# Optimization experiments

Hardware: AMD Instinct MI355X
Metric: run time of the kernel (lower is better)

The kernel has to match this reference:

```python
import math
import jax, jax.numpy as jnp
import numpy as np

B_, C_, K_, P_, STRIDE, ITERS = 32, 32, 3, 4, 2, 3
PSIZE = P_ * P_
EPS = 1e-8
LAM = 1e-3


def _unfold(x):
    # crude_convolution2d: gather-based unfold. x: (b, h, w, c)
    b, h, w, c = x.shape
    oh = int((h - K_ + 1) / STRIDE)
    idxs = np.array([[hi + k for k in range(K_)] for hi in range(0, h - K_ + 1, STRIDE)])  # (oh, K)
    x = x[:, idxs, :, :]        # (b, oh, K, w, c)
    x = x[:, :, :, idxs, :]     # (b, oh, K, ow, K, c)
    x = jnp.transpose(x, (0, 1, 3, 2, 4, 5))  # (b, oh, ow, K, K, c)
    return x, oh, oh


def _em_routing(v, a_in, beta_a, beta_u):
    # v: (n, Bk, C, psize), a_in: (n, Bk, 1). Standard matrix-capsule EM routing.
    n, Bk, C, psize = v.shape
    r = jnp.full((n, Bk, C), 1.0 / C, dtype=v.dtype)
    mu = a_out = None
    for it in range(ITERS):
        # M-step
        rr = r * a_in
        rr = rr / (jnp.sum(rr, axis=2, keepdims=True) + EPS)
        r_sum = jnp.sum(rr, axis=1, keepdims=True)              # (n, 1, C)
        coeff = (rr / (r_sum + EPS))[..., None]                 # (n, Bk, C, 1)
        mu = jnp.sum(coeff * v, axis=1, keepdims=True)          # (n, 1, C, psize)
        sigma_sq = jnp.sum(coeff * (v - mu) ** 2, axis=1, keepdims=True) + EPS
        log_sigma = 0.5 * jnp.log(sigma_sq)                     # log(sqrt(sigma_sq))
        cost_h = (beta_u[None, None, :, None] + log_sigma) * r_sum[..., None]
        a_out = jax.nn.sigmoid(LAM * (beta_a[None, None, :] - jnp.sum(cost_h, axis=3)))  # (n,1,C)
        if it < ITERS - 1:
            # E-step: Gaussian log-likelihood + log activation -> softmax over C
            ln_p = -(v - mu) ** 2 / (2.0 * sigma_sq) - log_sigma - 0.5 * math.log(2.0 * math.pi)
            ln_ap = jnp.sum(ln_p, axis=3) + jnp.log(a_out)      # (n, Bk, C)
            r = jax.nn.softmax(ln_ap, axis=2)
    return jnp.squeeze(mu, axis=1), jnp.squeeze(a_out, axis=1)


def setup_inputs() -> dict:
    key = jax.random.key(0)
    k1, k2 = jax.random.split(key)
    x = jax.random.uniform(k1, (8, 16, 16, B_ * (PSIZE + 1)), dtype=jnp.float32)
    weights = jax.random.normal(k2, (1, K_ * K_ * B_, C_, P_, P_), dtype=jnp.float32)
    beta_a = jnp.zeros((C_,), dtype=jnp.float32)
    beta_u = jnp.zeros((C_,), dtype=jnp.float32)
    return {"x": x, "weights": weights, "beta_a": beta_a, "beta_u": beta_u}


def reference(x, weights, beta_a, beta_u):
    b, h, w, c = x.shape
    xu, oh, ow = _unfold(x)                                   # (b, oh, ow, K, K, c)
    n = b * oh * ow
    p_in = xu[..., : B_ * PSIZE].reshape(n, K_ * K_ * B_, P_, P_)
    a_in = xu[..., B_ * PSIZE :].reshape(n, K_ * K_ * B_, 1)
    # transform_view: per (input-capsule k, output-capsule c) pose matmul
    v = jnp.einsum("nkij,kcjl->nkcil", p_in, weights[0]).reshape(n, K_ * K_ * B_, C_, PSIZE)
    mu, a_out = _em_routing(v, a_in, beta_a, beta_u)
    p_out = mu.reshape(b, oh, ow, C_ * PSIZE)
    a_out = a_out.reshape(b, oh, ow, C_)
    return jnp.concatenate([p_out, a_out], axis=3)
```

## Files before the change

kernel.cpp:

```cpp
#include <hip/hip_runtime.h>
#include <math.h>


#define NTH 512
#define KK 288
#define KSG 16
#define KT 18
#define CC 32
#define PS 16
#define EPSF 1e-8f
#define LAMF 1e-3f
#define HL2PI 0.91893853320467274178f
#define LOG2E 1.4426950408889634f

typedef float v2f __attribute__((ext_vector_type(2)));

__device__ __forceinline__ float4 ld4(const float* p){ return *(const float4*)p; }
__device__ __forceinline__ float rcpf(float x){ return __builtin_amdgcn_rcpf(x); }
__device__ __forceinline__ v2f bc2(float s){ return (v2f){s, s}; }
__device__ __forceinline__ v2f fma2(v2f a, v2f b, v2f c){ return __builtin_elementwise_fma(a, b, c); }

template<int CTRL>
__device__ __forceinline__ float dpp_add(float x){
  const int p = __builtin_amdgcn_update_dpp(0, __builtin_bit_cast(int, x),
                                            CTRL, 0xF, 0xF, true);
  return x + __builtin_bit_cast(float, p);
}
template<int CTRL>
__device__ __forceinline__ float dpp_max(float x){
  const int p = __builtin_amdgcn_update_dpp(0, __builtin_bit_cast(int, x),
                                            CTRL, 0xF, 0xF, true);
  return fmaxf(x, __builtin_bit_cast(float, p));
}
__device__ __forceinline__ float sum32(float s){
  s = dpp_add<0xB1>(s); s = dpp_add<0x4E>(s);
  s = dpp_add<0x141>(s); s = dpp_add<0x140>(s);
  s += __shfl_xor(s, 16);
  return s;
}

extern "C" __global__ void __launch_bounds__(NTH)
convcaps_em_kernel(const float* __restrict__ x, const float* __restrict__ wgt,
                   const float* __restrict__ beta_a, const float* __restrict__ beta_u,
                   float* __restrict__ out)
{
  __shared__ float sP[KK*PS];
  __shared__ float sA[KK];
  __shared__ float sPart[8*CC*33];
  __shared__ float sMu[CC*17];
  __shared__ float sNI2[CC*17];
  __shared__ float sLs[CC], sLnA[CC], sAo[CC];

  const int tid = threadIdx.x;
  const int n   = blockIdx.x;
  const int b   = n / 49;
  const int r49 = n - b*49;
  const int ohi = r49 / 7;
  const int owi = r49 - ohi*7;

  const float* xw = x + ((size_t)b*16 + (size_t)(ohi*2))*16*544 + (size_t)(owi*2)*544;

  const int c  = tid & 31;
  const int ks = tid >> 5;
  const int w  = tid >> 6;
  const int cc = tid >> 4;
  const int pp = tid & 15;

  for (int idx = tid; idx < KK*PS/4; idx += NTH) {
    const int sp  = idx >> 7;
    const int ch4 = idx & 127;
    const int kh = sp/3, kw = sp - kh*3;
    const float4 v = ld4(&xw[kh*(16*544) + kw*544 + ch4*4]);
    const int k = sp*32 + (ch4 >> 2);
    const int g = ch4 & 3;
    *(float4*)&sP[(k<<4) + ((g ^ ((k>>1)&3))<<2)] = v;
  }
  if (tid < KK/4) {
    const int sp  = tid >> 3;
    const int bc4 = tid & 7;
    const int kh = sp/3, kw = sp - kh*3;
    const float4 v = ld4(&xw[kh*(16*544) + kw*544 + 512 + bc4*4]);
    *(float4*)&sA[sp*32 + bc4*4] = v;
  }
  __syncthreads();
  if (tid < KK) { const float a = sA[tid]; sA[tid] = a * rcpf(a + EPSF); }
  __syncthreads();

  float t0;
  v2f t1[8], t2[8];

  auto stats = [&](){
    t0 += __shfl_xor(t0, 32);
#pragma unroll
    for (int q = 0; q < 8; ++q) {
      t1[q].x += __shfl_xor(t1[q].x, 32);
      t1[q].y += __shfl_xor(t1[q].y, 32);
      t2[q].x += __shfl_xor(t2[q].x, 32);
      t2[q].y += __shfl_xor(t2[q].y, 32);
    }
    if ((tid & 32) == 0) {
      float* pr = &sPart[(w*CC + c)*33];
      pr[0] = t0;
#pragma unroll
      for (int q = 0; q < 8; ++q) {
        pr[1 + 2*q]     = t1[q].x;  pr[1 + 2*q + 1]  = t1[q].y;
        pr[17 + 2*q]    = t2[q].x;  pr[17 + 2*q + 1] = t2[q].y;
      }
    }
    __syncthreads();
    {
      float T0 = 0.f, T1 = 0.f, T2 = 0.f;
#pragma unroll
      for (int j = 0; j < 8; ++j) {
        const float* pr = &sPart[(j*CC + cc)*33];
        T0 += pr[0]; T1 += pr[1+pp]; T2 += pr[17+pp];
      }
      const float z   = rcpf(T0 + EPSF);
      const float mu  = T1 * z;
      const float s0  = T0 * z;
      const float var = fmaxf(T2*z - mu*mu*(2.f - s0), 0.f) + EPSF;
      sMu[cc*17 + pp]  = mu;
      sNI2[cc*17 + pp] = -0.5f * rcpf(var);
      float lsum = 0.5f * __logf(var);
      lsum = dpp_add<0xB1>(lsum); lsum = dpp_add<0x4E>(lsum);
      lsum = dpp_add<0x141>(lsum); lsum = dpp_add<0x140>(lsum);
      if (pp == 0) {
        const float cost = (16.f*beta_u[cc] + lsum) * T0;
        const float ao = rcpf(1.f + __expf(-(LAMF*(beta_a[cc] - cost))));
        sAo[cc] = ao; sLnA[cc] = __logf(ao); sLs[cc] = lsum;
      }
    }
    __syncthreads();
  };

  const float4* wg4 = (const float4*)wgt;

  auto compute_v = [&](v2f (&v)[8], const float4 (&P)[4],
                       const float4& W0, const float4& W1,
                       const float4& W2, const float4& W3){
    const v2f w0lo = {W0.x,W0.y}, w0hi = {W0.z,W0.w};
    const v2f w1lo = {W1.x,W1.y}, w1hi = {W1.z,W1.w};
    const v2f w2lo = {W2.x,W2.y}, w2hi = {W2.z,W2.w};
    const v2f w3lo = {W3.x,W3.y}, w3hi = {W3.z,W3.w};
#pragma unroll
    for (int i = 0; i < 4; ++i) {
      v2f lo = bc2(P[i].x) * w0lo;
      lo = fma2(bc2(P[i].y), w1lo, lo);
      lo = fma2(bc2(P[i].z), w2lo, lo);
      lo = fma2(bc2(P[i].w), w3lo, lo);
      v2f hi = bc2(P[i].x) * w0hi;
      hi = fma2(bc2(P[i].y), w1hi, hi);
      hi = fma2(bc2(P[i].z), w2hi, hi);
      hi = fma2(bc2(P[i].w), w3hi, hi);
      v[i*2] = lo; v[i*2+1] = hi;
    }
  };

  t0 = 0.f;
#pragma unroll
  for (int q = 0; q < 8; ++q) { t1[q] = bc2(0.f); t2[q] = bc2(0.f); }
  {
    float4 cw0, cw1, cw2, cw3;
    {
      const size_t base = ((size_t)(ks*32 + c))*4;
      cw0 = wg4[base]; cw1 = wg4[base+1]; cw2 = wg4[base+2]; cw3 = wg4[base+3];
    }
#pragma unroll 1
    for (int kt = 0; kt < KT; ++kt) {
      const int k = kt*KSG + ks;
      const int kn = ((kt+1 < KT) ? kt+1 : kt)*KSG + ks;
      float4 nw0, nw1, nw2, nw3;
      {
        const size_t base = ((size_t)(kn*32 + c))*4;
        nw0 = wg4[base]; nw1 = wg4[base+1]; nw2 = wg4[base+2]; nw3 = wg4[base+3];
      }
      const v2f w0lo = {cw0.x,cw0.y}, w0hi = {cw0.z,cw0.w};
      const v2f w1lo = {cw1.x,cw1.y}, w1hi = {cw1.z,cw1.w};
      const v2f w2lo = {cw2.x,cw2.y}, w2hi = {cw2.z,cw2.w};
      const v2f w3lo = {cw3.x,cw3.y}, w3hi = {cw3.z,cw3.w};
      const int sw = (k>>1)&3;
      const float* pb = &sP[k<<4];
      const float4 Pi[4] = { ld4(pb + ((0^sw)<<2)), ld4(pb + ((1^sw)<<2)),
                             ld4(pb + ((2^sw)<<2)), ld4(pb + ((3^sw)<<2)) };
      const float rr = sA[k] * (1.0f/32.0f);
      t0 += rr;
      const v2f rr2 = bc2(rr);
#pragma unroll
      for (int i = 0; i < 4; ++i) {
        v2f lo = bc2(Pi[i].x) * w0lo;
        lo = fma2(bc2(Pi[i].y), w1lo, lo);
        lo = fma2(bc2(Pi[i].z), w2lo, lo);
        lo = fma2(bc2(Pi[i].w), w3lo, lo);
        v2f hi = bc2(Pi[i].x) * w0hi;
        hi = fma2(bc2(Pi[i].y), w1hi, hi);
        hi = fma2(bc2(Pi[i].z), w2hi, hi);
        hi = fma2(bc2(Pi[i].w), w3hi, hi);
        const v2f mlo = rr2 * lo, mhi = rr2 * hi;
        t1[i*2]   += mlo;  t2[i*2]   = fma2(mlo, lo, t2[i*2]);
        t1[i*2+1] += mhi;  t2[i*2+1] = fma2(mhi, hi, t2[i*2+1]);
      }
      cw0 = nw0; cw1 = nw1; cw2 = nw2; cw3 = nw3;
    }
  }
  stats();

  for (int it = 1; it < 3; ++it) {
    v2f A2[8], B2[8];
    float gsum = 0.f;
#pragma unroll
    for (int q = 0; q < 8; ++q) {
      const v2f m2 = (v2f){ sMu[c*17 + 2*q],  sMu[c*17 + 2*q + 1] };
      const v2f n2 = (v2f){ sNI2[c*17 + 2*q], sNI2[c*17 + 2*q + 1] };
      const v2f nm = n2 * m2;
      A2[q] = bc2(LOG2E) * n2;
      B2[q] = bc2(-2.f*LOG2E) * nm;
      const v2f g2 = nm * m2;
      gsum += g2.x + g2.y;
    }
    float lcv = sLnA[c] - sLs[c] - 16.f*HL2PI;
    float M = lcv;
    M = dpp_max<0xB1>(M);  M = dpp_max<0x4E>(M);
    M = dpp_max<0x141>(M); M = dpp_max<0x140>(M);
    M = fmaxf(M, __shfl_xor(M, 16));
    const float G = LOG2E*(gsum + lcv - M);

    auto softmax_moments = [&](const v2f (&v)[8], float fA){
      v2f acc2 = bc2(0.f);
#pragma unroll
      for (int q = 0; q < 8; ++q) {
        const v2f h = fma2(A2[q], v[q], B2[q]);
        acc2 = fma2(h, v[q], acc2);
      }
      const float ex = acc2.x + acc2.y + G;
      const float e = exp2f(ex);
      const float s = sum32(e);
      const float rr = e * rcpf(s + 1e-37f) * fA;
      t0 += rr;
      const v2f rr2 = bc2(rr);
#pragma unroll
      for (int q = 0; q < 8; ++q) {
        const v2f tmp = rr2 * v[q];
        t1[q] += tmp;
        t2[q] = fma2(tmp, v[q], t2[q]);
      }
    };

    t0 = 0.f;
#pragma unroll
    for (int q = 0; q < 8; ++q) { t1[q] = bc2(0.f); t2[q] = bc2(0.f); }

    v2f vA[8];
    {
      const int k = ks;
      const size_t base = ((size_t)(k*32 + c))*4;
      const float4 w0 = wg4[base], w1 = wg4[base+1], w2 = wg4[base+2], w3 = wg4[base+3];
      const int sw = (k>>1)&3;
      const float* pb = &sP[k<<4];
      const float4 Pi[4] = { ld4(pb + ((0^sw)<<2)), ld4(pb + ((1^sw)<<2)),
                             ld4(pb + ((2^sw)<<2)), ld4(pb + ((3^sw)<<2)) };
      compute_v(vA, Pi, w0, w1, w2, w3);
    }
#pragma unroll 1
    for (int kt = 1; kt < KT; ++kt) {
      const int k  = kt*KSG + ks;
      const int kp = k - KSG;
      const size_t base = ((size_t)(k*32 + c))*4;
      const float4 w0 = wg4[base], w1 = wg4[base+1], w2 = wg4[base+2], w3 = wg4[base+3];
      const float fA = sA[kp];
      const int sw = (k>>1)&3;
      const float* pb = &sP[k<<4];
      const float4 Pi[4] = { ld4(pb + ((0^sw)<<2)), ld4(pb + ((1^sw)<<2)),
                             ld4(pb + ((2^sw)<<2)), ld4(pb + ((3^sw)<<2)) };
      softmax_moments(vA, fA);
      compute_v(vA, Pi, w0, w1, w2, w3);
    }
    softmax_moments(vA, sA[(KT-1)*KSG + ks]);
    stats();
  }

  out[(size_t)n*544 + tid] = sMu[(tid>>4)*17 + (tid&15)];
  if (tid < CC) out[(size_t)n*544 + 512 + tid] = sAo[tid];
}

extern "C" void kernel_launch(void* const* d_in, const int* in_sizes, int n_in,
                              void* d_out, int out_size, void* d_ws, size_t ws_size,
                              hipStream_t stream) {
  (void)in_sizes; (void)n_in; (void)d_ws; (void)ws_size; (void)out_size;
  const float* x  = (const float*)d_in[0];
  const float* w  = (const float*)d_in[1];
  const float* ba = (const float*)d_in[2];
  const float* bu = (const float*)d_in[3];
  float* out = (float*)d_out;
  convcaps_em_kernel<<<dim3(392), dim3(NTH), 0, stream>>>(x, w, ba, bu, out);
}
```

Before: 120.3 us.

## Software-pipeline the E-step softmax reduction against moment accumulation across tiles

The E-step loop is restructured into a two-buffer software pipeline. While the cross-lane softmax sum for the current tile is in flight, the moment accumulation for the previous tile runs, followed by computing the next tile's votes. The quadratic-form accumulation is also split into two independent accumulators to shorten the FMA dependency chain. The cost is an extra set of vote registers held live, which raises register pressure and could lower occupancy or cause spills.

```diff
diff --git a/kernel.cpp b/kernel.cpp
--- a/kernel.cpp
+++ b/kernel.cpp
@@ -224,17 +224,21 @@
     M = fmaxf(M, __shfl_xor(M, 16));
     const float G = LOG2E*(gsum + lcv - M);
 
-    auto softmax_moments = [&](const v2f (&v)[8], float fA){
-      v2f acc2 = bc2(0.f);
-#pragma unroll
-      for (int q = 0; q < 8; ++q) {
-        const v2f h = fma2(A2[q], v[q], B2[q]);
-        acc2 = fma2(h, v[q], acc2);
-      }
-      const float ex = acc2.x + acc2.y + G;
-      const float e = exp2f(ex);
-      const float s = sum32(e);
-      const float rr = e * rcpf(s + 1e-37f) * fA;
+    t0 = 0.f;
+#pragma unroll
+    for (int q = 0; q < 8; ++q) { t1[q] = bc2(0.f); t2[q] = bc2(0.f); }
+
+    auto quad_e = [&](const v2f (&v)[8]) -> float {
+      v2f accA = bc2(0.f), accB = bc2(0.f);
+#pragma unroll
+      for (int q = 0; q < 8; q += 2) {
+        accA = fma2(fma2(A2[q],   v[q],   B2[q]),   v[q],   accA);
+        accB = fma2(fma2(A2[q+1], v[q+1], B2[q+1]), v[q+1], accB);
+      }
+      const float ex = (accA.x + accA.y) + (accB.x + accB.y) + G;
+      return exp2f(ex);
+    };
+    auto moments = [&](const v2f (&v)[8], float rr){
       t0 += rr;
       const v2f rr2 = bc2(rr);
 #pragma unroll
@@ -245,11 +249,24 @@
       }
     };
 
-    t0 = 0.f;
-#pragma unroll
-    for (int q = 0; q < 8; ++q) { t1[q] = bc2(0.f); t2[q] = bc2(0.f); }
-
-    v2f vA[8];
+    float rrPrev = 0.f;
+    auto bodyD = [&](v2f (&vP)[8], v2f (&vO)[8], const int t){
+      const int kn = t*KSG + ks;
+      const size_t base = ((size_t)(kn*32 + c))*4;
+      const float4 w0 = wg4[base], w1 = wg4[base+1], w2 = wg4[base+2], w3 = wg4[base+3];
+      const float fA = sA[(t-1)*KSG + ks];
+      const int sw = (kn>>1)&3;
+      const float* pb = &sP[kn<<4];
+      const float4 Pi[4] = { ld4(pb + ((0^sw)<<2)), ld4(pb + ((1^sw)<<2)),
+                             ld4(pb + ((2^sw)<<2)), ld4(pb + ((3^sw)<<2)) };
+      const float e = quad_e(vP);
+      const float s = sum32(e);
+      moments(vO, rrPrev);
+      rrPrev = e * rcpf(s + 1e-37f) * fA;
+      compute_v(vO, Pi, w0, w1, w2, w3);
+    };
+
+    v2f va[8], vb[8];
     {
       const int k = ks;
       const size_t base = ((size_t)(k*32 + c))*4;
@@ -258,23 +275,35 @@
       const float* pb = &sP[k<<4];
       const float4 Pi[4] = { ld4(pb + ((0^sw)<<2)), ld4(pb + ((1^sw)<<2)),
                              ld4(pb + ((2^sw)<<2)), ld4(pb + ((3^sw)<<2)) };
-      compute_v(vA, Pi, w0, w1, w2, w3);
-    }
-#pragma unroll 1
-    for (int kt = 1; kt < KT; ++kt) {
-      const int k  = kt*KSG + ks;
-      const int kp = k - KSG;
-      const size_t base = ((size_t)(k*32 + c))*4;
+      compute_v(va, Pi, w0, w1, w2, w3);
+    }
+    {
+      const int kn = KSG + ks;
+      const size_t base = ((size_t)(kn*32 + c))*4;
       const float4 w0 = wg4[base], w1 = wg4[base+1], w2 = wg4[base+2], w3 = wg4[base+3];
-      const float fA = sA[kp];
-      const int sw = (k>>1)&3;
-      const float* pb = &sP[k<<4];
+      const float fA = sA[ks];
+      const int sw = (kn>>1)&3;
+      const float* pb = &sP[kn<<4];
       const float4 Pi[4] = { ld4(pb + ((0^sw)<<2)), ld4(pb + ((1^sw)<<2)),
                              ld4(pb + ((2^sw)<<2)), ld4(pb + ((3^sw)<<2)) };
-      softmax_moments(vA, fA);
-      compute_v(vA, Pi, w0, w1, w2, w3);
-    }
-    softmax_moments(vA, sA[(KT-1)*KSG + ks]);
+      const float e = quad_e(va);
+      const float s = sum32(e);
+      rrPrev = e * rcpf(s + 1e-37f) * fA;
+      compute_v(vb, Pi, w0, w1, w2, w3);
+    }
+#pragma unroll 1
+    for (int t = 2; t + 1 < KT; t += 2) {
+      bodyD(vb, va, t);
+      bodyD(va, vb, t + 1);
+    }
+    {
+      const float fA = sA[(KT-1)*KSG + ks];
+      const float e = quad_e(vb);
+      const float s = sum32(e);
+      moments(va, rrPrev);
+      const float rrL = e * rcpf(s + 1e-37f) * fA;
+      moments(vb, rrL);
+    }
     stats();
   }
 
```

After: 120.3 us. No clear change (-0.0%).
